# Kernel optimization log

Hardware: AMD Instinct MI355X
Metric: run time of the kernel (lower is better)

Reference implementation:

```python
import jax, jax.numpy as jnp
import numpy as np

SL, BS, HS, FFN = 2048, 1, 512, 2048
E, TOP_K = 8, 2


def setup_inputs() -> dict:
    key = jax.random.key(0)
    k_x, k_w, k_i, k_w1, k_w2 = jax.random.split(key, 5)
    x = jax.random.normal(k_x, (SL, BS, HS), dtype=jnp.float32)
    expert_weights = jax.random.uniform(k_w, (SL * BS, TOP_K), dtype=jnp.float32)
    expert_indices = jax.random.randint(k_i, (SL * BS, TOP_K), 0, E, dtype=jnp.int32)
    # grouped expert MLP params (megablocks GroupedMLP, regular type, no bias)
    w1 = jax.random.normal(k_w1, (E, HS, FFN), dtype=jnp.float32) * (HS ** -0.5)
    w2 = jax.random.normal(k_w2, (E, FFN, HS), dtype=jnp.float32) * (FFN ** -0.5)
    return {"x": x, "expert_weights": expert_weights, "expert_indices": expert_indices,
            "w1": w1, "w2": w2}


def reference(x, expert_weights, expert_indices, w1, w2):
    sl, bs, hs = x.shape
    n_tok = sl * bs
    xf = x.reshape(n_tok, hs)                      # [N, hs]
    ew = expert_weights.reshape(-1)                # [N*top_k]
    ei = expert_indices.reshape(-1)                # [N*top_k]

    # indices_and_bins: stable radix sort of assignments by expert id
    indices = jnp.argsort(ei)                      # stable in jax -> sorted assignment ids
    bin_ids = ei[indices]                          # sorted expert id per assignment

    # megablocks gather: row for assignment i is indices[i] // top_k
    rows = indices // TOP_K                        # [T]
    xg = xf[rows]                                  # [T, hs] expert-contiguous tokens

    # grouped GEMM expert MLP (dense masked loop over fixed expert count)
    outg = jnp.zeros_like(xg)
    for e in range(E):
        m = (bin_ids == e).astype(x.dtype)[:, None]
        h = jax.nn.gelu(xg @ w1[e], approximate=False)   # [T, ffn]
        outg = outg + m * (h @ w2[e])                    # [T, hs]

    # buffer.index_add_(0, E*input_indices + bin_ids, output.detach())
    buf_idx = E * rows + bin_ids
    buffer = jnp.zeros((n_tok * E, hs), x.dtype).at[buf_idx].add(
        jax.lax.stop_gradient(outg))

    # megablocks scatter: weighted combine back to token order
    y = jnp.zeros((n_tok, hs), x.dtype).at[rows].add(outg * ew[indices][:, None])
    return y.reshape(sl, bs, hs), buffer.reshape(n_tok, E, hs)
```

## Files before the change

kernel.cpp:

```cpp
#include <hip/hip_runtime.h>
#include <hip/hip_bf16.h>

#define NTOK 2048
#define TOPK 2
#define HS   512
#define FFN  2048
#define NE   8
#define TASSIGN (NTOK*TOPK)
#define PAD  5120
#define MAXT128 40
#define MAXT64  72

typedef __attribute__((ext_vector_type(8))) short bf16x8;
typedef __attribute__((ext_vector_type(8))) unsigned short u16x8;
typedef __attribute__((ext_vector_type(4))) float f32x4;

static const size_t OFF_XBF  = 0;
static const size_t OFF_W1T  = 2097152;
static const size_t OFF_W2T  = 18874368;
static const size_t OFF_H    = 35651584;
static const size_t OFF_OUTV = 56623104;
static const size_t OFF_RT   = 67108864;
static const size_t OFF_HROF = 67129344;
static const size_t OFF_TE128= 67145728;
static const size_t OFF_TR128= 67145888;
static const size_t OFF_TE64 = 67146048;
static const size_t OFF_TR64 = 67146336;

__device__ __forceinline__ unsigned short f2bf(float f) {
    union { __hip_bfloat16 h; unsigned short u; } v;
    v.h = __float2bfloat16(f);
    return v.u;
}

__device__ __forceinline__ float bf2f(unsigned short u) {
    union { unsigned int i; float f; } v;
    v.i = ((unsigned int)u) << 16;
    return v.f;
}

__device__ __forceinline__ int swz(int r, int byte_off) {
    return byte_off ^ ((r & 7) << 4);
}

__device__ __forceinline__ float gelu_fast(float x) {
    float z2 = x * fmaf(0.0713548162726f, x * x, 1.5957691216057f);
    float e = __expf(z2);
    return x - __fdividef(x, e + 1.0f);
}

#define GLOAD16(gsrc, ldst) \
    __builtin_amdgcn_global_load_lds((const __attribute__((address_space(1))) void*)(gsrc), \
                                     (__attribute__((address_space(3))) void*)(ldst), 16, 0, 0)

__device__ __forceinline__ void dev_transpose(const float* __restrict__ in,
                                              unsigned short* __restrict__ out,
                                              int R, int C, int e, int rb, int cb, int tid) {
    __shared__ unsigned short t[32][33];
    int tx = tid & 31, ty = tid >> 5;
    const float* ip = in + (size_t)e * R * C;
    unsigned short* op = out + (size_t)e * C * R;
#pragma unroll
    for (int i = 0; i < 4; i++) {
        int r = ty + i * 8;
        t[r][tx] = f2bf(ip[(size_t)(rb + r) * C + cb + tx]);
    }
    __syncthreads();
#pragma unroll
    for (int i = 0; i < 4; i++) {
        int c = ty + i * 8;
        op[(size_t)(cb + c) * R + rb + tx] = t[tx][c];
    }
}

__global__ __launch_bounds__(256) void k_prep(
        const float* __restrict__ x, const float* __restrict__ w1,
        const float* __restrict__ w2, const int* __restrict__ ei,
        unsigned short* __restrict__ xbf, unsigned short* __restrict__ w1T,
        unsigned short* __restrict__ w2T,
        int* __restrict__ rowtok, int* __restrict__ hrof,
        int* __restrict__ te128, int* __restrict__ tr128,
        int* __restrict__ te64, int* __restrict__ tr64) {
    int b = blockIdx.x;
    int tid = threadIdx.x;
    if (b == 0) {
        __shared__ int cnt[NE], offpad[NE], cur[NE];
        for (int i = tid; i < PAD; i += 256) rowtok[i] = 0;
        if (tid < NE) cnt[tid] = 0;
        __syncthreads();
        for (int a = tid; a < TASSIGN; a += 256) atomicAdd(&cnt[ei[a]], 1);
        __syncthreads();
        if (tid == 0) {
            int o = 0, t1 = 0, t2 = 0;
            for (int e = 0; e < NE; e++) {
                offpad[e] = o; cur[e] = 0;
                for (int r = 0; r < cnt[e]; r += 128) { te128[t1] = e; tr128[t1] = o + r; t1++; }
                for (int r = 0; r < cnt[e]; r += 64)  { te64[t2]  = e; tr64[t2]  = o + r; t2++; }
                o += (cnt[e] + 127) / 128 * 128;
            }
            for (; t1 < MAXT128; t1++) te128[t1] = -1;
            for (; t2 < MAXT64;  t2++) te64[t2]  = -1;
        }
        __syncthreads();
        for (int a = tid; a < TASSIGN; a += 256) {
            int e = ei[a];
            int r = atomicAdd(&cur[e], 1);
            int hr = offpad[e] + r;
            rowtok[hr] = a >> 1;
            hrof[a] = hr;
        }
    } else if (b < 1 + 1024) {
        int i = ((b - 1) * 256 + tid) * 4;
        float4 v = *(const float4*)(x + i);
        ushort4 o;
        o.x = f2bf(v.x); o.y = f2bf(v.y); o.z = f2bf(v.z); o.w = f2bf(v.w);
        *(ushort4*)(xbf + i) = o;
    } else if (b < 1 + 1024 + 8192) {
        int blk = b - 1025;
        int e = blk >> 10, rem = blk & 1023;
        dev_transpose(w1, w1T, HS, FFN, e, (rem >> 6) * 32, (rem & 63) * 32, tid);
    } else {
        int blk = b - 9217;
        int e = blk >> 10, rem = blk & 1023;
        dev_transpose(w2, w2T, FFN, HS, e, (rem >> 4) * 32, (rem & 15) * 32, tid);
    }
}

template<int BM, int BN, int KFULL, int KLOC, bool G1>
__global__ __launch_bounds__(256) void k_gemm(
        const unsigned short* __restrict__ A,
        const unsigned short* __restrict__ B,
        unsigned short* __restrict__ outp,
        const int* __restrict__ rowtok,
        const int* __restrict__ te, const int* __restrict__ tr, int N) {
    constexpr int MI = BM / 32, NJ = BN / 32;
    constexpr int PA = BM / 32, PB = BN / 32;
    constexpr int ABYTES = BM * 64 * 2, BBYTES = BN * 64 * 2;
    constexpr int NSTEP = KLOC / 64;
    static_assert(NSTEP % 2 == 0 && NSTEP >= 4, "even steps >= 4");

    int mt = blockIdx.y;
    int e = te[mt];
    if (e < 0) return;
    int hr0 = tr[mt];
    int ct = blockIdx.x;
    int kz = blockIdx.z;
    int k0 = kz * KLOC;

    __shared__ int4 ldsv[(2 * (ABYTES + BBYTES)) / 16];
    char* A0 = (char*)ldsv;
    char* A1 = A0 + ABYTES;
    char* B0 = A1 + ABYTES;
    char* B1 = B0 + BBYTES;

    int tid = threadIdx.x;
    int lane = tid & 63, wave = tid >> 6;
    int wm = wave >> 1, wn = wave & 1;

    const char* asrc[PA];
    const char* bsrc[PB];
    int adoff[PA], bdoff[PB];
#pragma unroll
    for (int p = 0; p < PA; p++) {
        int idx = p * 256 + tid;
        int r = idx >> 3, c8 = idx & 7;
        int c8s = c8 ^ (r & 7);
        size_t row = G1 ? (size_t)rowtok[hr0 + r] : (size_t)(hr0 + r);
        asrc[p] = (const char*)(A + row * KFULL + k0) + c8s * 16;
        adoff[p] = (p * 256 + wave * 64) * 16;
    }
#pragma unroll
    for (int p = 0; p < PB; p++) {
        int idx = p * 256 + tid;
        int r = idx >> 3, c8 = idx & 7;
        int c8s = c8 ^ (r & 7);
        bsrc[p] = (const char*)(B + ((size_t)e * N + (size_t)ct * BN + r) * KFULL + k0) + c8s * 16;
        bdoff[p] = (p * 256 + wave * 64) * 16;
    }

    f32x4 acc[MI][NJ] = {};

    auto stage = [&](char* Ad, char* Bd, int s) {
        int kb = s * 128;
#pragma unroll
        for (int p = 0; p < PA; p++) GLOAD16(asrc[p] + kb, Ad + adoff[p]);
#pragma unroll
        for (int p = 0; p < PB; p++) GLOAD16(bsrc[p] + kb, Bd + bdoff[p]);
    };
    auto compute = [&](const char* As, const char* Bs) {
#pragma unroll
        for (int kk = 0; kk < 64; kk += 32) {
            bf16x8 af[MI], bfv[NJ];
#pragma unroll
            for (int i = 0; i < MI; i++) {
                int ar = wm * (BM / 2) + i * 16 + (lane & 15);
                af[i] = *(const bf16x8*)(As + swz(ar, ar * 128 + kk * 2 + (lane >> 4) * 16));
            }
#pragma unroll
            for (int j = 0; j < NJ; j++) {
                int bc = wn * (BN / 2) + j * 16 + (lane & 15);
                bfv[j] = *(const bf16x8*)(Bs + swz(bc, bc * 128 + kk * 2 + (lane >> 4) * 16));
            }
#pragma unroll
            for (int i = 0; i < MI; i++)
#pragma unroll
                for (int j = 0; j < NJ; j++)
                    acc[i][j] = __builtin_amdgcn_mfma_f32_16x16x32_bf16(af[i], bfv[j], acc[i][j], 0, 0, 0);
        }
    };
    auto waitv_lps = [&]() {
        if constexpr (PA + PB == 6)      { asm volatile("s_waitcnt vmcnt(6)" ::: "memory"); }
        else if constexpr (PA + PB == 4) { asm volatile("s_waitcnt vmcnt(4)" ::: "memory"); }
        else                             { asm volatile("s_waitcnt vmcnt(0)" ::: "memory"); }
    };
    auto waitv0 = [&]() { asm volatile("s_waitcnt vmcnt(0)" ::: "memory"); };
    auto waitlgkm = [&]() { asm volatile("s_waitcnt lgkmcnt(0)" ::: "memory"); };
    auto bar = [&]() {
        __builtin_amdgcn_sched_barrier(0);
        __builtin_amdgcn_s_barrier();
        __builtin_amdgcn_sched_barrier(0);
        asm volatile("" ::: "memory");
    };

    stage(A0, B0, 0);
    stage(A1, B1, 1);
#pragma unroll 1
    for (int s = 0; s + 2 < NSTEP; s += 2) {
        waitv_lps(); bar();
        compute(A0, B0);
        waitlgkm(); bar();
        stage(A0, B0, s + 2);
        waitv_lps(); bar();
        compute(A1, B1);
        waitlgkm(); bar();
        if (s + 3 < NSTEP) stage(A1, B1, s + 3);
    }
    waitv_lps(); bar();
    compute(A0, B0);
    waitv0(); bar();
    compute(A1, B1);

    if constexpr (G1) {
#pragma unroll
        for (int i = 0; i < MI; i++)
#pragma unroll
            for (int j = 0; j < NJ; j++)
#pragma unroll
                for (int q = 0; q < 4; q++) {
                    int row = hr0 + wm * (BM / 2) + i * 16 + (lane >> 4) * 4 + q;
                    int col = ct * BN + wn * (BN / 2) + j * 16 + (lane & 15);
                    outp[(size_t)row * N + col] = f2bf(gelu_fast(acc[i][j][q]));
                }
    } else {
        unsigned short* O = outp + (size_t)kz * PAD * HS;
#pragma unroll
        for (int i = 0; i < MI; i++)
#pragma unroll
            for (int j = 0; j < NJ; j++)
#pragma unroll
                for (int q = 0; q < 4; q++) {
                    int row = hr0 + wm * (BM / 2) + i * 16 + (lane >> 4) * 4 + q;
                    int col = ct * BN + wn * (BN / 2) + j * 16 + (lane & 15);
                    O[(size_t)row * N + col] = f2bf(acc[i][j][q]);
                }
    }
}

__global__ __launch_bounds__(256) void k_combine(
        const unsigned short* __restrict__ outv, const int* __restrict__ ei,
        const float* __restrict__ ew, const int* __restrict__ hrof,
        float* __restrict__ y, float* __restrict__ buf) {
    constexpr size_t SPLIT = (size_t)PAD * HS;
    int g = blockIdx.x * 256 + threadIdx.x;
    int t = g >> 6, c8 = g & 63;
    int a0 = 2 * t, a1 = a0 + 1;
    int h0 = hrof[a0], h1 = hrof[a1];
    u16x8 q0a = *(const u16x8*)(outv + (size_t)h0 * HS + c8 * 8);
    u16x8 q0b = *(const u16x8*)(outv + SPLIT + (size_t)h0 * HS + c8 * 8);
    u16x8 q1a = *(const u16x8*)(outv + (size_t)h1 * HS + c8 * 8);
    u16x8 q1b = *(const u16x8*)(outv + SPLIT + (size_t)h1 * HS + c8 * 8);
    float w0 = ew[a0], w1 = ew[a1];
    float o0[8], o1[8], yy[8];
#pragma unroll
    for (int k = 0; k < 8; k++) {
        o0[k] = bf2f(q0a[k]) + bf2f(q0b[k]);
        o1[k] = bf2f(q1a[k]) + bf2f(q1b[k]);
        yy[k] = w0 * o0[k] + w1 * o1[k];
    }
    float* yp = y + (size_t)t * HS + c8 * 8;
    *(float4*)(yp)     = make_float4(yy[0], yy[1], yy[2], yy[3]);
    *(float4*)(yp + 4) = make_float4(yy[4], yy[5], yy[6], yy[7]);
    int e0 = ei[a0], e1 = ei[a1];
    float* bt = buf + (size_t)t * (NE * HS) + c8 * 8;
#pragma unroll
    for (int e = 0; e < NE; e++) {
        float v[8];
#pragma unroll
        for (int k = 0; k < 8; k++)
            v[k] = (e == e0 ? o0[k] : 0.0f) + (e == e1 ? o1[k] : 0.0f);
        float* be = bt + (size_t)e * HS;
        *(float4*)(be)     = make_float4(v[0], v[1], v[2], v[3]);
        *(float4*)(be + 4) = make_float4(v[4], v[5], v[6], v[7]);
    }
}

extern "C" void kernel_launch(void* const* d_in, const int* in_sizes, int n_in,
                              void* d_out, int out_size, void* d_ws, size_t ws_size,
                              hipStream_t stream) {
    const float* x  = (const float*)d_in[0];
    const float* ew = (const float*)d_in[1];
    const int*   ei = (const int*)d_in[2];
    const float* w1 = (const float*)d_in[3];
    const float* w2 = (const float*)d_in[4];

    char* ws = (char*)d_ws;
    unsigned short* xbf  = (unsigned short*)(ws + OFF_XBF);
    unsigned short* w1T  = (unsigned short*)(ws + OFF_W1T);
    unsigned short* w2T  = (unsigned short*)(ws + OFF_W2T);
    unsigned short* Hb   = (unsigned short*)(ws + OFF_H);
    unsigned short* outv = (unsigned short*)(ws + OFF_OUTV);
    int*            rowtok = (int*)(ws + OFF_RT);
    int*            hrof   = (int*)(ws + OFF_HROF);
    int*            te128  = (int*)(ws + OFF_TE128);
    int*            tr128  = (int*)(ws + OFF_TR128);
    int*            te64   = (int*)(ws + OFF_TE64);
    int*            tr64   = (int*)(ws + OFF_TR64);

    float* y   = (float*)d_out;
    float* buf = (float*)d_out + (size_t)NTOK * HS;

    k_prep<<<1 + 1024 + 8192 + 8192, 256, 0, stream>>>(
        x, w1, w2, ei, xbf, w1T, w2T, rowtok, hrof, te128, tr128, te64, tr64);
    k_gemm<128, 64, HS, HS, true><<<dim3(FFN / 64, MAXT128), 256, 0, stream>>>(
        xbf, w1T, Hb, rowtok, te128, tr128, FFN);
    k_gemm<64, 64, FFN, FFN / 2, false><<<dim3(HS / 64, MAXT64, 2), 256, 0, stream>>>(
        Hb, w2T, outv, rowtok, te64, tr64, HS);
    k_combine<<<NTOK * HS / 8 / 256, 256, 0, stream>>>(
        outv, ei, ew, hrof, y, buf);
}
```

Before: 83.95 us.

## Fuse fp32 weight conversion and transpose into GEMM B-tile loading

Drops the separate pass that turned w1 and w2 into transposed bf16 copies in the prep kernel. Each GEMM now reads fp32 weights straight from global memory into registers, converts them to bf16 and writes them transposed into a new swizzled LDS layout, one stage ahead through register double buffering. This removes a large extra read and write of both weight tensors. In exchange, every M tile re-reads and re-converts fp32 weights at twice the bytes, uses more registers, and the async LDS pipeline for B is replaced by register staging; compute also gains s_setprio.

Result: slower. 87.48 us (+4.2%).

```diff
diff --git a/kernel.cpp b/kernel.cpp
--- a/kernel.cpp
+++ b/kernel.cpp
@@ -16,16 +16,14 @@
 typedef __attribute__((ext_vector_type(4))) float f32x4;
 
 static const size_t OFF_XBF  = 0;
-static const size_t OFF_W1T  = 2097152;
-static const size_t OFF_W2T  = 18874368;
-static const size_t OFF_H    = 35651584;
-static const size_t OFF_OUTV = 56623104;
-static const size_t OFF_RT   = 67108864;
-static const size_t OFF_HROF = 67129344;
-static const size_t OFF_TE128= 67145728;
-static const size_t OFF_TR128= 67145888;
-static const size_t OFF_TE64 = 67146048;
-static const size_t OFF_TR64 = 67146336;
+static const size_t OFF_H    = 2097152;
+static const size_t OFF_OUTV = 23068672;
+static const size_t OFF_RT   = 33554432;
+static const size_t OFF_HROF = 33574912;
+static const size_t OFF_TE128= 33591296;
+static const size_t OFF_TR128= 33591456;
+static const size_t OFF_TE64 = 33591616;
+static const size_t OFF_TR64 = 33591904;
 
 __device__ __forceinline__ unsigned short f2bf(float f) {
     union { __hip_bfloat16 h; unsigned short u; } v;
@@ -39,8 +37,11 @@
     return v.f;
 }
 
-__device__ __forceinline__ int swz(int r, int byte_off) {
+__device__ __forceinline__ int swza(int r, int byte_off) {
     return byte_off ^ ((r & 7) << 4);
+}
+__device__ __forceinline__ int swzb(int n, int byte_off) {
+    return byte_off ^ ((((n & 7) ^ ((n >> 2) & 7))) << 4);
 }
 
 __device__ __forceinline__ float gelu_fast(float x) {
@@ -53,31 +54,9 @@
     __builtin_amdgcn_global_load_lds((const __attribute__((address_space(1))) void*)(gsrc), \
                                      (__attribute__((address_space(3))) void*)(ldst), 16, 0, 0)
 
-__device__ __forceinline__ void dev_transpose(const float* __restrict__ in,
-                                              unsigned short* __restrict__ out,
-                                              int R, int C, int e, int rb, int cb, int tid) {
-    __shared__ unsigned short t[32][33];
-    int tx = tid & 31, ty = tid >> 5;
-    const float* ip = in + (size_t)e * R * C;
-    unsigned short* op = out + (size_t)e * C * R;
-#pragma unroll
-    for (int i = 0; i < 4; i++) {
-        int r = ty + i * 8;
-        t[r][tx] = f2bf(ip[(size_t)(rb + r) * C + cb + tx]);
-    }
-    __syncthreads();
-#pragma unroll
-    for (int i = 0; i < 4; i++) {
-        int c = ty + i * 8;
-        op[(size_t)(cb + c) * R + rb + tx] = t[tx][c];
-    }
-}
-
 __global__ __launch_bounds__(256) void k_prep(
-        const float* __restrict__ x, const float* __restrict__ w1,
-        const float* __restrict__ w2, const int* __restrict__ ei,
-        unsigned short* __restrict__ xbf, unsigned short* __restrict__ w1T,
-        unsigned short* __restrict__ w2T,
+        const float* __restrict__ x, const int* __restrict__ ei,
+        unsigned short* __restrict__ xbf,
         int* __restrict__ rowtok, int* __restrict__ hrof,
         int* __restrict__ te128, int* __restrict__ tr128,
         int* __restrict__ te64, int* __restrict__ tr64) {
@@ -109,34 +88,28 @@
             rowtok[hr] = a >> 1;
             hrof[a] = hr;
         }
-    } else if (b < 1 + 1024) {
+    } else {
         int i = ((b - 1) * 256 + tid) * 4;
         float4 v = *(const float4*)(x + i);
         ushort4 o;
         o.x = f2bf(v.x); o.y = f2bf(v.y); o.z = f2bf(v.z); o.w = f2bf(v.w);
         *(ushort4*)(xbf + i) = o;
-    } else if (b < 1 + 1024 + 8192) {
-        int blk = b - 1025;
-        int e = blk >> 10, rem = blk & 1023;
-        dev_transpose(w1, w1T, HS, FFN, e, (rem >> 6) * 32, (rem & 63) * 32, tid);
-    } else {
-        int blk = b - 9217;
-        int e = blk >> 10, rem = blk & 1023;
-        dev_transpose(w2, w2T, FFN, HS, e, (rem >> 4) * 32, (rem & 15) * 32, tid);
     }
 }
 
 template<int BM, int BN, int KFULL, int KLOC, bool G1>
 __global__ __launch_bounds__(256) void k_gemm(
         const unsigned short* __restrict__ A,
-        const unsigned short* __restrict__ B,
+        const float* __restrict__ W,
         unsigned short* __restrict__ outp,
         const int* __restrict__ rowtok,
         const int* __restrict__ te, const int* __restrict__ tr, int N) {
     constexpr int MI = BM / 32, NJ = BN / 32;
-    constexpr int PA = BM / 32, PB = BN / 32;
-    constexpr int ABYTES = BM * 64 * 2, BBYTES = BN * 64 * 2;
+    constexpr int PA = BM / 32;
+    constexpr int ABYTES = BM * 64 * 2;
+    constexpr int BBYTES = 64 * 64 * 2;
     constexpr int NSTEP = KLOC / 64;
+    static_assert(BN == 64, "BN fixed at 64");
     static_assert(NSTEP % 2 == 0 && NSTEP >= 4, "even steps >= 4");
 
     int mt = blockIdx.y;
@@ -147,7 +120,7 @@
     int kz = blockIdx.z;
     int k0 = kz * KLOC;
 
-    __shared__ int4 ldsv[(2 * (ABYTES + BBYTES)) / 16];
+    __shared__ int4 ldsv[(2 * ABYTES + 2 * BBYTES) / 16];
     char* A0 = (char*)ldsv;
     char* A1 = A0 + ABYTES;
     char* B0 = A1 + ABYTES;
@@ -158,8 +131,7 @@
     int wm = wave >> 1, wn = wave & 1;
 
     const char* asrc[PA];
-    const char* bsrc[PB];
-    int adoff[PA], bdoff[PB];
+    int adoff[PA];
 #pragma unroll
     for (int p = 0; p < PA; p++) {
         int idx = p * 256 + tid;
@@ -169,37 +141,61 @@
         asrc[p] = (const char*)(A + row * KFULL + k0) + c8s * 16;
         adoff[p] = (p * 256 + wave * 64) * 16;
     }
-#pragma unroll
-    for (int p = 0; p < PB; p++) {
-        int idx = p * 256 + tid;
-        int r = idx >> 3, c8 = idx & 7;
-        int c8s = c8 ^ (r & 7);
-        bsrc[p] = (const char*)(B + ((size_t)e * N + (size_t)ct * BN + r) * KFULL + k0) + c8s * 16;
-        bdoff[p] = (p * 256 + wave * 64) * 16;
-    }
+    int n0 = (tid & 15) * 4;
+    int k0t = (tid >> 4) * 4;
+    const float* bsrcf = W + ((size_t)e * KFULL + (size_t)(k0 + k0t)) * N
+                           + (size_t)ct * BN + n0;
 
     f32x4 acc[MI][NJ] = {};
-
-    auto stage = [&](char* Ad, char* Bd, int s) {
+    float4 bregE[4], bregO[4];
+
+    auto issueA = [&](int s, char* Ad) {
         int kb = s * 128;
 #pragma unroll
         for (int p = 0; p < PA; p++) GLOAD16(asrc[p] + kb, Ad + adoff[p]);
-#pragma unroll
-        for (int p = 0; p < PB; p++) GLOAD16(bsrc[p] + kb, Bd + bdoff[p]);
+    };
+    auto issueB = [&](int s, float4* br) {
+        const float* p = bsrcf + (size_t)s * 64 * N;
+#pragma unroll
+        for (int j = 0; j < 4; j++) br[j] = *(const float4*)(p + (size_t)j * N);
+    };
+    auto cvtwrite = [&](float4* br, char* Bd) {
+        float4 b0 = br[0], b1 = br[1], b2 = br[2], b3 = br[3];
+        unsigned long long v0 = (unsigned long long)f2bf(b0.x)
+            | ((unsigned long long)f2bf(b1.x) << 16)
+            | ((unsigned long long)f2bf(b2.x) << 32)
+            | ((unsigned long long)f2bf(b3.x) << 48);
+        unsigned long long v1 = (unsigned long long)f2bf(b0.y)
+            | ((unsigned long long)f2bf(b1.y) << 16)
+            | ((unsigned long long)f2bf(b2.y) << 32)
+            | ((unsigned long long)f2bf(b3.y) << 48);
+        unsigned long long v2 = (unsigned long long)f2bf(b0.z)
+            | ((unsigned long long)f2bf(b1.z) << 16)
+            | ((unsigned long long)f2bf(b2.z) << 32)
+            | ((unsigned long long)f2bf(b3.z) << 48);
+        unsigned long long v3 = (unsigned long long)f2bf(b0.w)
+            | ((unsigned long long)f2bf(b1.w) << 16)
+            | ((unsigned long long)f2bf(b2.w) << 32)
+            | ((unsigned long long)f2bf(b3.w) << 48);
+        *(unsigned long long*)(Bd + swzb(n0 + 0, (n0 + 0) * 128 + k0t * 2)) = v0;
+        *(unsigned long long*)(Bd + swzb(n0 + 1, (n0 + 1) * 128 + k0t * 2)) = v1;
+        *(unsigned long long*)(Bd + swzb(n0 + 2, (n0 + 2) * 128 + k0t * 2)) = v2;
+        *(unsigned long long*)(Bd + swzb(n0 + 3, (n0 + 3) * 128 + k0t * 2)) = v3;
     };
     auto compute = [&](const char* As, const char* Bs) {
+        __builtin_amdgcn_s_setprio(1);
 #pragma unroll
         for (int kk = 0; kk < 64; kk += 32) {
             bf16x8 af[MI], bfv[NJ];
 #pragma unroll
             for (int i = 0; i < MI; i++) {
                 int ar = wm * (BM / 2) + i * 16 + (lane & 15);
-                af[i] = *(const bf16x8*)(As + swz(ar, ar * 128 + kk * 2 + (lane >> 4) * 16));
+                af[i] = *(const bf16x8*)(As + swza(ar, ar * 128 + kk * 2 + (lane >> 4) * 16));
             }
 #pragma unroll
             for (int j = 0; j < NJ; j++) {
                 int bc = wn * (BN / 2) + j * 16 + (lane & 15);
-                bfv[j] = *(const bf16x8*)(Bs + swz(bc, bc * 128 + kk * 2 + (lane >> 4) * 16));
+                bfv[j] = *(const bf16x8*)(Bs + swzb(bc, bc * 128 + kk * 2 + (lane >> 4) * 16));
             }
 #pragma unroll
             for (int i = 0; i < MI; i++)
@@ -207,14 +203,9 @@
                 for (int j = 0; j < NJ; j++)
                     acc[i][j] = __builtin_amdgcn_mfma_f32_16x16x32_bf16(af[i], bfv[j], acc[i][j], 0, 0, 0);
         }
-    };
-    auto waitv_lps = [&]() {
-        if constexpr (PA + PB == 6)      { asm volatile("s_waitcnt vmcnt(6)" ::: "memory"); }
-        else if constexpr (PA + PB == 4) { asm volatile("s_waitcnt vmcnt(4)" ::: "memory"); }
-        else                             { asm volatile("s_waitcnt vmcnt(0)" ::: "memory"); }
-    };
-    auto waitv0 = [&]() { asm volatile("s_waitcnt vmcnt(0)" ::: "memory"); };
-    auto waitlgkm = [&]() { asm volatile("s_waitcnt lgkmcnt(0)" ::: "memory"); };
+        __builtin_amdgcn_s_setprio(0);
+    };
+    auto lgkm0 = [&]() { asm volatile("s_waitcnt lgkmcnt(0)" ::: "memory"); };
     auto bar = [&]() {
         __builtin_amdgcn_sched_barrier(0);
         __builtin_amdgcn_s_barrier();
@@ -222,22 +213,27 @@
         asm volatile("" ::: "memory");
     };
 
-    stage(A0, B0, 0);
-    stage(A1, B1, 1);
+    issueA(0, A0); issueB(0, bregE);
+    issueA(1, A1); issueB(1, bregO);
+    cvtwrite(bregE, B0);
+    lgkm0(); bar();
+    compute(A0, B0);
 #pragma unroll 1
-    for (int s = 0; s + 2 < NSTEP; s += 2) {
-        waitv_lps(); bar();
+    for (int s = 1; s + 1 < NSTEP; s += 2) {
+        bar();
+        issueA(s + 1, A0); issueB(s + 1, bregE);
+        cvtwrite(bregO, B1);
+        lgkm0(); bar();
+        compute(A1, B1);
+        bar();
+        issueA(s + 2, A1); issueB(s + 2, bregO);
+        cvtwrite(bregE, B0);
+        lgkm0(); bar();
         compute(A0, B0);
-        waitlgkm(); bar();
-        stage(A0, B0, s + 2);
-        waitv_lps(); bar();
-        compute(A1, B1);
-        waitlgkm(); bar();
-        if (s + 3 < NSTEP) stage(A1, B1, s + 3);
-    }
-    waitv_lps(); bar();
-    compute(A0, B0);
-    waitv0(); bar();
+    }
+    bar();
+    cvtwrite(bregO, B1);
+    lgkm0(); bar();
     compute(A1, B1);
 
     if constexpr (G1) {
@@ -315,8 +311,6 @@
 
     char* ws = (char*)d_ws;
     unsigned short* xbf  = (unsigned short*)(ws + OFF_XBF);
-    unsigned short* w1T  = (unsigned short*)(ws + OFF_W1T);
-    unsigned short* w2T  = (unsigned short*)(ws + OFF_W2T);
     unsigned short* Hb   = (unsigned short*)(ws + OFF_H);
     unsigned short* outv = (unsigned short*)(ws + OFF_OUTV);
     int*            rowtok = (int*)(ws + OFF_RT);
@@ -329,12 +323,12 @@
     float* y   = (float*)d_out;
     float* buf = (float*)d_out + (size_t)NTOK * HS;
 
-    k_prep<<<1 + 1024 + 8192 + 8192, 256, 0, stream>>>(
-        x, w1, w2, ei, xbf, w1T, w2T, rowtok, hrof, te128, tr128, te64, tr64);
+    k_prep<<<1 + 1024, 256, 0, stream>>>(
+        x, ei, xbf, rowtok, hrof, te128, tr128, te64, tr64);
     k_gemm<128, 64, HS, HS, true><<<dim3(FFN / 64, MAXT128), 256, 0, stream>>>(
-        xbf, w1T, Hb, rowtok, te128, tr128, FFN);
+        xbf, w1, Hb, rowtok, te128, tr128, FFN);
     k_gemm<64, 64, FFN, FFN / 2, false><<<dim3(HS / 64, MAXT64, 2), 256, 0, stream>>>(
-        Hb, w2T, outv, rowtok, te64, tr64, HS);
+        Hb, w2, outv, rowtok, te64, tr64, HS);
     k_combine<<<NTOK * HS / 8 / 256, 256, 0, stream>>>(
         outv, ei, ew, hrof, y, buf);
 }
```

## Move w2 transpose into tail of first GEMM with vectorized tiles

Applied to the files above, without the earlier changes.

The w2 fp32→bf16 transpose leaves the prep kernel. It now runs as a grid-strided tail inside the first grouped GEMM kernel, including blocks with no expert work, so it overlaps with GEMM1 compute instead of running serially before it. The transpose also switches to 32x64 tiles with float4 loads and ushort4 stores, cutting the number of blocks and memory transactions. The cost is more LDS reuse and barriers in GEMM1 blocks, plus a longer tail for the blocks that run GEMM work.

New measurement: 87.25 us. 1.04x slower.

```diff
diff --git a/kernel.cpp b/kernel.cpp
--- a/kernel.cpp
+++ b/kernel.cpp
@@ -73,11 +73,35 @@
     }
 }
 
+__device__ __forceinline__ void dev_tr2(const float* __restrict__ in,
+                                        unsigned short* __restrict__ out,
+                                        int R, int C, int e, int rb, int cb,
+                                        int tid, unsigned short* t) {
+    const float* ip = in + (size_t)e * R * C + (size_t)rb * C + cb;
+    unsigned short* op = out + (size_t)e * C * R + (size_t)cb * R + rb;
+    int r = tid >> 3, c8 = (tid & 7) * 8;
+    float4 v0 = *(const float4*)(ip + (size_t)r * C + c8);
+    float4 v1 = *(const float4*)(ip + (size_t)r * C + c8 + 4);
+    ushort4 lo, hi;
+    lo.x = f2bf(v0.x); lo.y = f2bf(v0.y); lo.z = f2bf(v0.z); lo.w = f2bf(v0.w);
+    hi.x = f2bf(v1.x); hi.y = f2bf(v1.y); hi.z = f2bf(v1.z); hi.w = f2bf(v1.w);
+    *(ushort4*)(t + r * 72 + c8)     = lo;
+    *(ushort4*)(t + r * 72 + c8 + 4) = hi;
+    __syncthreads();
+    int c = tid >> 2, r8 = (tid & 3) * 8;
+    ushort4 a, b;
+    a.x = t[(r8 + 0) * 72 + c]; a.y = t[(r8 + 1) * 72 + c];
+    a.z = t[(r8 + 2) * 72 + c]; a.w = t[(r8 + 3) * 72 + c];
+    b.x = t[(r8 + 4) * 72 + c]; b.y = t[(r8 + 5) * 72 + c];
+    b.z = t[(r8 + 6) * 72 + c]; b.w = t[(r8 + 7) * 72 + c];
+    *(ushort4*)(op + (size_t)c * R + r8)     = a;
+    *(ushort4*)(op + (size_t)c * R + r8 + 4) = b;
+}
+
 __global__ __launch_bounds__(256) void k_prep(
         const float* __restrict__ x, const float* __restrict__ w1,
-        const float* __restrict__ w2, const int* __restrict__ ei,
+        const int* __restrict__ ei,
         unsigned short* __restrict__ xbf, unsigned short* __restrict__ w1T,
-        unsigned short* __restrict__ w2T,
         int* __restrict__ rowtok, int* __restrict__ hrof,
         int* __restrict__ te128, int* __restrict__ tr128,
         int* __restrict__ te64, int* __restrict__ tr64) {
@@ -115,154 +139,167 @@
         ushort4 o;
         o.x = f2bf(v.x); o.y = f2bf(v.y); o.z = f2bf(v.z); o.w = f2bf(v.w);
         *(ushort4*)(xbf + i) = o;
-    } else if (b < 1 + 1024 + 8192) {
+    } else {
         int blk = b - 1025;
         int e = blk >> 10, rem = blk & 1023;
         dev_transpose(w1, w1T, HS, FFN, e, (rem >> 6) * 32, (rem & 63) * 32, tid);
-    } else {
-        int blk = b - 9217;
-        int e = blk >> 10, rem = blk & 1023;
-        dev_transpose(w2, w2T, FFN, HS, e, (rem >> 4) * 32, (rem & 15) * 32, tid);
-    }
-}
-
-template<int BM, int BN, int KFULL, int KLOC, bool G1>
+    }
+}
+
+template<int BM, int BN, int KFULL, int KLOC, bool G1, bool W2TAIL>
 __global__ __launch_bounds__(256) void k_gemm(
         const unsigned short* __restrict__ A,
         const unsigned short* __restrict__ B,
         unsigned short* __restrict__ outp,
         const int* __restrict__ rowtok,
-        const int* __restrict__ te, const int* __restrict__ tr, int N) {
+        const int* __restrict__ te, const int* __restrict__ tr, int N,
+        const float* __restrict__ w2, unsigned short* __restrict__ w2T) {
     constexpr int MI = BM / 32, NJ = BN / 32;
     constexpr int PA = BM / 32, PB = BN / 32;
     constexpr int ABYTES = BM * 64 * 2, BBYTES = BN * 64 * 2;
     constexpr int NSTEP = KLOC / 64;
     static_assert(NSTEP % 2 == 0 && NSTEP >= 4, "even steps >= 4");
 
+    __shared__ int4 ldsv[(2 * (ABYTES + BBYTES)) / 16];
+    int tid = threadIdx.x;
+
     int mt = blockIdx.y;
     int e = te[mt];
-    if (e < 0) return;
-    int hr0 = tr[mt];
-    int ct = blockIdx.x;
-    int kz = blockIdx.z;
-    int k0 = kz * KLOC;
-
-    __shared__ int4 ldsv[(2 * (ABYTES + BBYTES)) / 16];
-    char* A0 = (char*)ldsv;
-    char* A1 = A0 + ABYTES;
-    char* B0 = A1 + ABYTES;
-    char* B1 = B0 + BBYTES;
-
-    int tid = threadIdx.x;
-    int lane = tid & 63, wave = tid >> 6;
-    int wm = wave >> 1, wn = wave & 1;
-
-    const char* asrc[PA];
-    const char* bsrc[PB];
-    int adoff[PA], bdoff[PB];
-#pragma unroll
-    for (int p = 0; p < PA; p++) {
-        int idx = p * 256 + tid;
-        int r = idx >> 3, c8 = idx & 7;
-        int c8s = c8 ^ (r & 7);
-        size_t row = G1 ? (size_t)rowtok[hr0 + r] : (size_t)(hr0 + r);
-        asrc[p] = (const char*)(A + row * KFULL + k0) + c8s * 16;
-        adoff[p] = (p * 256 + wave * 64) * 16;
-    }
-#pragma unroll
-    for (int p = 0; p < PB; p++) {
-        int idx = p * 256 + tid;
-        int r = idx >> 3, c8 = idx & 7;
-        int c8s = c8 ^ (r & 7);
-        bsrc[p] = (const char*)(B + ((size_t)e * N + (size_t)ct * BN + r) * KFULL + k0) + c8s * 16;
-        bdoff[p] = (p * 256 + wave * 64) * 16;
-    }
-
-    f32x4 acc[MI][NJ] = {};
-
-    auto stage = [&](char* Ad, char* Bd, int s) {
-        int kb = s * 128;
-#pragma unroll
-        for (int p = 0; p < PA; p++) GLOAD16(asrc[p] + kb, Ad + adoff[p]);
-#pragma unroll
-        for (int p = 0; p < PB; p++) GLOAD16(bsrc[p] + kb, Bd + bdoff[p]);
-    };
-    auto compute = [&](const char* As, const char* Bs) {
-#pragma unroll
-        for (int kk = 0; kk < 64; kk += 32) {
-            bf16x8 af[MI], bfv[NJ];
-#pragma unroll
-            for (int i = 0; i < MI; i++) {
-                int ar = wm * (BM / 2) + i * 16 + (lane & 15);
-                af[i] = *(const bf16x8*)(As + swz(ar, ar * 128 + kk * 2 + (lane >> 4) * 16));
+    if (e >= 0) {
+        int hr0 = tr[mt];
+        int ct = blockIdx.x;
+        int kz = blockIdx.z;
+        int k0 = kz * KLOC;
+
+        char* A0 = (char*)ldsv;
+        char* A1 = A0 + ABYTES;
+        char* B0 = A1 + ABYTES;
+        char* B1 = B0 + BBYTES;
+
+        int lane = tid & 63, wave = tid >> 6;
+        int wm = wave >> 1, wn = wave & 1;
+
+        const char* asrc[PA];
+        const char* bsrc[PB];
+        int adoff[PA], bdoff[PB];
+#pragma unroll
+        for (int p = 0; p < PA; p++) {
+            int idx = p * 256 + tid;
+            int r = idx >> 3, c8 = idx & 7;
+            int c8s = c8 ^ (r & 7);
+            size_t row = G1 ? (size_t)rowtok[hr0 + r] : (size_t)(hr0 + r);
+            asrc[p] = (const char*)(A + row * KFULL + k0) + c8s * 16;
+            adoff[p] = (p * 256 + wave * 64) * 16;
+        }
+#pragma unroll
+        for (int p = 0; p < PB; p++) {
+            int idx = p * 256 + tid;
+            int r = idx >> 3, c8 = idx & 7;
+            int c8s = c8 ^ (r & 7);
+            bsrc[p] = (const char*)(B + ((size_t)e * N + (size_t)ct * BN + r) * KFULL + k0) + c8s * 16;
+            bdoff[p] = (p * 256 + wave * 64) * 16;
+        }
+
+        f32x4 acc[MI][NJ] = {};
+
+        auto stage = [&](char* Ad, char* Bd, int s) {
+            int kb = s * 128;
+#pragma unroll
+            for (int p = 0; p < PA; p++) GLOAD16(asrc[p] + kb, Ad + adoff[p]);
+#pragma unroll
+            for (int p = 0; p < PB; p++) GLOAD16(bsrc[p] + kb, Bd + bdoff[p]);
+        };
+        auto compute = [&](const char* As, const char* Bs) {
+#pragma unroll
+            for (int kk = 0; kk < 64; kk += 32) {
+                bf16x8 af[MI], bfv[NJ];
+#pragma unroll
+                for (int i = 0; i < MI; i++) {
+                    int ar = wm * (BM / 2) + i * 16 + (lane & 15);
+                    af[i] = *(const bf16x8*)(As + swz(ar, ar * 128 + kk * 2 + (lane >> 4) * 16));
+                }
+#pragma unroll
+                for (int j = 0; j < NJ; j++) {
+                    int bc = wn * (BN / 2) + j * 16 + (lane & 15);
+                    bfv[j] = *(const bf16x8*)(Bs + swz(bc, bc * 128 + kk * 2 + (lane >> 4) * 16));
+                }
+#pragma unroll
+                for (int i = 0; i < MI; i++)
+#pragma unroll
+                    for (int j = 0; j < NJ; j++)
+                        acc[i][j] = __builtin_amdgcn_mfma_f32_16x16x32_bf16(af[i], bfv[j], acc[i][j], 0, 0, 0);
             }
-#pragma unroll
-            for (int j = 0; j < NJ; j++) {
-                int bc = wn * (BN / 2) + j * 16 + (lane & 15);
-                bfv[j] = *(const bf16x8*)(Bs + swz(bc, bc * 128 + kk * 2 + (lane >> 4) * 16));
-            }
-#pragma unroll
-            for (int i = 0; i < MI; i++)
-#pragma unroll
-                for (int j = 0; j < NJ; j++)
-                    acc[i][j] = __builtin_amdgcn_mfma_f32_16x16x32_bf16(af[i], bfv[j], acc[i][j], 0, 0, 0);
-        }
-    };
-    auto waitv_lps = [&]() {
-        if constexpr (PA + PB == 6)      { asm volatile("s_waitcnt vmcnt(6)" ::: "memory"); }
-        else if constexpr (PA + PB == 4) { asm volatile("s_waitcnt vmcnt(4)" ::: "memory"); }
-        else                             { asm volatile("s_waitcnt vmcnt(0)" ::: "memory"); }
-    };
-    auto waitv0 = [&]() { asm volatile("s_waitcnt vmcnt(0)" ::: "memory"); };
-    auto waitlgkm = [&]() { asm volatile("s_waitcnt lgkmcnt(0)" ::: "memory"); };
-    auto bar = [&]() {
-        __builtin_amdgcn_sched_barrier(0);
-        __builtin_amdgcn_s_barrier();
-        __builtin_amdgcn_sched_barrier(0);
-        asm volatile("" ::: "memory");
-    };
-
-    stage(A0, B0, 0);
-    stage(A1, B1, 1);
+        };
+        auto waitv_lps = [&]() {
+            if constexpr (PA + PB == 6)      { asm volatile("s_waitcnt vmcnt(6)" ::: "memory"); }
+            else if constexpr (PA + PB == 4) { asm volatile("s_waitcnt vmcnt(4)" ::: "memory"); }
+            else                             { asm volatile("s_waitcnt vmcnt(0)" ::: "memory"); }
+        };
+        auto waitv0 = [&]() { asm volatile("s_waitcnt vmcnt(0)" ::: "memory"); };
+        auto waitlgkm = [&]() { asm volatile("s_waitcnt lgkmcnt(0)" ::: "memory"); };
+        auto bar = [&]() {
+            __builtin_amdgcn_sched_barrier(0);
+            __builtin_amdgcn_s_barrier();
+            __builtin_amdgcn_sched_barrier(0);
+            asm volatile("" ::: "memory");
+        };
+
+        stage(A0, B0, 0);
+        stage(A1, B1, 1);
 #pragma unroll 1
-    for (int s = 0; s + 2 < NSTEP; s += 2) {
+        for (int s = 0; s + 2 < NSTEP; s += 2) {
+            waitv_lps(); bar();
+            compute(A0, B0);
+            waitlgkm(); bar();
+            stage(A0, B0, s + 2);
+            waitv_lps(); bar();
+            compute(A1, B1);
+            waitlgkm(); bar();
+            if (s + 3 < NSTEP) stage(A1, B1, s + 3);
+        }
         waitv_lps(); bar();
         compute(A0, B0);
-        waitlgkm(); bar();
-        stage(A0, B0, s + 2);
-        waitv_lps(); bar();
+        waitv0(); bar();
         compute(A1, B1);
-        waitlgkm(); bar();
-        if (s + 3 < NSTEP) stage(A1, B1, s + 3);
-    }
-    waitv_lps(); bar();
-    compute(A0, B0);
-    waitv0(); bar();
-    compute(A1, B1);
-
-    if constexpr (G1) {
-#pragma unroll
-        for (int i = 0; i < MI; i++)
-#pragma unroll
-            for (int j = 0; j < NJ; j++)
-#pragma unroll
-                for (int q = 0; q < 4; q++) {
-                    int row = hr0 + wm * (BM / 2) + i * 16 + (lane >> 4) * 4 + q;
-                    int col = ct * BN + wn * (BN / 2) + j * 16 + (lane & 15);
-                    outp[(size_t)row * N + col] = f2bf(gelu_fast(acc[i][j][q]));
-                }
-    } else {
-        unsigned short* O = outp + (size_t)kz * PAD * HS;
-#pragma unroll
-        for (int i = 0; i < MI; i++)
-#pragma unroll
-            for (int j = 0; j < NJ; j++)
-#pragma unroll
-                for (int q = 0; q < 4; q++) {
-                    int row = hr0 + wm * (BM / 2) + i * 16 + (lane >> 4) * 4 + q;
-                    int col = ct * BN + wn * (BN / 2) + j * 16 + (lane & 15);
-                    O[(size_t)row * N + col] = f2bf(acc[i][j][q]);
-                }
+
+        if constexpr (G1) {
+#pragma unroll
+            for (int i = 0; i < MI; i++)
+#pragma unroll
+                for (int j = 0; j < NJ; j++)
+#pragma unroll
+                    for (int q = 0; q < 4; q++) {
+                        int row = hr0 + wm * (BM / 2) + i * 16 + (lane >> 4) * 4 + q;
+                        int col = ct * BN + wn * (BN / 2) + j * 16 + (lane & 15);
+                        outp[(size_t)row * N + col] = f2bf(gelu_fast(acc[i][j][q]));
+                    }
+        } else {
+            unsigned short* O = outp + (size_t)kz * PAD * HS;
+#pragma unroll
+            for (int i = 0; i < MI; i++)
+#pragma unroll
+                for (int j = 0; j < NJ; j++)
+#pragma unroll
+                    for (int q = 0; q < 4; q++) {
+                        int row = hr0 + wm * (BM / 2) + i * 16 + (lane >> 4) * 4 + q;
+                        int col = ct * BN + wn * (BN / 2) + j * 16 + (lane & 15);
+                        O[(size_t)row * N + col] = f2bf(acc[i][j][q]);
+                    }
+        }
+    }
+
+    if constexpr (W2TAIL) {
+        __builtin_amdgcn_s_barrier();
+        unsigned short* tsh = (unsigned short*)ldsv;
+        int bid = blockIdx.y * gridDim.x + blockIdx.x;
+        int nblk = gridDim.x * gridDim.y;
+#pragma unroll 1
+        for (int t = bid; t < NE * (FFN / 32) * (HS / 64); t += nblk) {
+            __syncthreads();
+            int e2 = t >> 9;
+            int rem = t & 511;
+            dev_tr2(w2, w2T, FFN, HS, e2, (rem >> 3) * 32, (rem & 7) * 64, tid, tsh);
+        }
     }
 }
 
@@ -329,12 +366,12 @@
     float* y   = (float*)d_out;
     float* buf = (float*)d_out + (size_t)NTOK * HS;
 
-    k_prep<<<1 + 1024 + 8192 + 8192, 256, 0, stream>>>(
-        x, w1, w2, ei, xbf, w1T, w2T, rowtok, hrof, te128, tr128, te64, tr64);
-    k_gemm<128, 64, HS, HS, true><<<dim3(FFN / 64, MAXT128), 256, 0, stream>>>(
-        xbf, w1T, Hb, rowtok, te128, tr128, FFN);
-    k_gemm<64, 64, FFN, FFN / 2, false><<<dim3(HS / 64, MAXT64, 2), 256, 0, stream>>>(
-        Hb, w2T, outv, rowtok, te64, tr64, HS);
+    k_prep<<<1 + 1024 + 8192, 256, 0, stream>>>(
+        x, w1, ei, xbf, w1T, rowtok, hrof, te128, tr128, te64, tr64);
+    k_gemm<128, 64, HS, HS, true, true><<<dim3(FFN / 64, MAXT128), 256, 0, stream>>>(
+        xbf, w1T, Hb, rowtok, te128, tr128, FFN, w2, w2T);
+    k_gemm<64, 64, FFN, FFN / 2, false, false><<<dim3(HS / 64, MAXT64, 2), 256, 0, stream>>>(
+        Hb, w2T, outv, rowtok, te64, tr64, HS, nullptr, nullptr);
     k_combine<<<NTOK * HS / 8 / 256, 256, 0, stream>>>(
         outv, ei, ew, hrof, y, buf);
 }
```
